# Kernel optimization log

Hardware: AMD Instinct MI355X
Metric: run time of the kernel (lower is better)

## Reference

```python
import jax, jax.numpy as jnp
import numpy as np

V, D, H, NH, C, L = 11, 128, 256, 4, 10, 3  # vocab, d_model, ffn/out dim, heads, classes, layers
DH = D // NH


def setup_inputs() -> dict:
    key = jax.random.key(0)
    ks = jax.random.split(key, 12)
    s = 0.02
    return {
        "support_inputs": jax.random.randint(ks[0], (64, 1024), 0, 11),
        "support_outputs": jax.random.randint(ks[1], (64, 1024), 0, 10),
        "query_input": jax.random.randint(ks[2], (1024,), 0, 11),
        "support_masks": jax.random.randint(ks[3], (64, 1024), 0, 2),
        "emb": (jax.random.normal(ks[4], (V, D)) * s).at[10].set(0.0),  # padding_idx=10
        "Wqkv": jax.random.normal(ks[5], (L, 3 * D, D)) * s,
        "bqkv": jnp.zeros((L, 3 * D)),
        "Wo": jax.random.normal(ks[6], (L, D, D)) * s,
        "bo": jnp.zeros((L, D)),
        "ln1_s": jnp.ones((L, D)), "ln1_b": jnp.zeros((L, D)),
        "W1": jax.random.normal(ks[7], (L, H, D)) * s, "b1": jnp.zeros((L, H)),
        "W2": jax.random.normal(ks[8], (L, D, H)) * s, "b2": jnp.zeros((L, D)),
        "ln2_s": jnp.ones((L, D)), "ln2_b": jnp.zeros((L, D)),
        "Wp": jax.random.normal(ks[9], (H, D)) * s, "bp": jnp.zeros((H,)),
    }


def _ln(x, s, b, eps=1e-5):
    m = x.mean(-1, keepdims=True)
    v = ((x - m) ** 2).mean(-1, keepdims=True)
    return (x - m) / jnp.sqrt(v + eps) * s + b


def _encode(tokens, emb, Wqkv, bqkv, Wo, bo, ln1_s, ln1_b, W1, b1, W2, b2, ln2_s, ln2_b, Wp, bp):
    # PyTorch TransformerEncoderLayer, post-norm (norm_first=False), relu, eval (no dropout)
    x = emb[tokens]  # [B, S, D]
    B, S, _ = x.shape
    scale = 1.0 / jnp.sqrt(jnp.asarray(DH, x.dtype))
    for l in range(L):
        qkv = jnp.einsum('bsd,ed->bse', x, Wqkv[l]) + bqkv[l]
        q, k, v = jnp.split(qkv, 3, axis=-1)
        q = q.reshape(B, S, NH, DH)
        k = k.reshape(B, S, NH, DH)
        v = v.reshape(B, S, NH, DH)
        scores = jnp.einsum('bqhd,bkhd->bhqk', q, k) * scale
        a = jax.nn.softmax(scores, axis=-1)
        o = jnp.einsum('bhqk,bkhd->bqhd', a, v).reshape(B, S, D)
        o = o @ Wo[l].T + bo[l]
        x = _ln(x + o, ln1_s[l], ln1_b[l])
        f = jax.nn.relu(x @ W1[l].T + b1[l]) @ W2[l].T + b2[l]
        x = _ln(x + f, ln2_s[l], ln2_b[l])
    return x @ Wp.T + bp  # [B, S, H]


def reference(support_inputs, support_outputs, query_input, support_masks,
              emb, Wqkv, bqkv, Wo, bo, ln1_s, ln1_b, W1, b1, W2, b2, ln2_s, ln2_b, Wp, bp):
    params = (emb, Wqkv, bqkv, Wo, bo, ln1_s, ln1_b, W1, b1, W2, b2, ln2_s, ln2_b, Wp, bp)
    feat = _encode(support_inputs, *params)  # [N, S, H]
    # vectorized scatter-mean: invalid (masked or cls>=C) tokens go to dummy segment C
    seg = jnp.where((support_masks > 0) & (support_outputs < C), support_outputs, C).reshape(-1)
    flat = feat.reshape(-1, H)
    sums = jax.ops.segment_sum(flat, seg, num_segments=C + 1)[:C]
    cnts = jax.ops.segment_sum(jnp.ones((seg.shape[0],), flat.dtype), seg, num_segments=C + 1)[:C]
    protos = jnp.where(cnts[:, None] > 0, sums / jnp.maximum(cnts, 1.0)[:, None], 0.0)  # [C, H]
    qf = _encode(query_input[None, :], *params)[0]  # [S, H]
    logits = -jnp.sum((qf[:, None, :] - protos[None, :, :]) ** 2, axis=-1)  # -cdist**2, [S, C]
    return logits
```

## Files before the change

### kernel.cpp

```cpp
#include <hip/hip_runtime.h>
#include <hip/hip_bf16.h>

constexpr int D    = 128;
constexpr int HF   = 256;
constexpr int NH   = 4;
constexpr int DH   = 32;
constexpr int NL   = 3;
constexpr int SEQ  = 1024;
constexpr int NB   = 65;
constexpr int NTOK = NB * SEQ;
constexpr int NSUP = 64 * SEQ;
constexpr int NC   = 10;

using u16 = unsigned short;
using u32 = unsigned int;
typedef __bf16 bf16x8 __attribute__((ext_vector_type(8)));
typedef float  f32x4  __attribute__((ext_vector_type(4)));
typedef float  f32x16 __attribute__((ext_vector_type(16)));
typedef u16    u16x4  __attribute__((ext_vector_type(4)));
typedef u16    u16x8  __attribute__((ext_vector_type(8)));
typedef u32    u32x2  __attribute__((ext_vector_type(2)));

static __device__ __forceinline__ u16 f2b(float f) {
  return __builtin_bit_cast(u16, (__bf16)f);
}
static __device__ __forceinline__ float b2f(u16 u) {
  return (float)__builtin_bit_cast(__bf16, u);
}

#define GLOAD16(gsrc, ldst) \
  __builtin_amdgcn_global_load_lds( \
      (const __attribute__((address_space(1))) void*)(gsrc), \
      (__attribute__((address_space(3))) void*)(ldst), 16, 0, 0)

__global__ __launch_bounds__(256) void k_setup(const float* __restrict__ w0,
                                               const float* __restrict__ w1,
                                               const float* __restrict__ w2,
                                               const float* __restrict__ w3,
                                               const float* __restrict__ w4,
                                               u16* __restrict__ wout,
                                               const int* __restrict__ sup,
                                               const int* __restrict__ qry,
                                               const float* __restrict__ emb,
                                               u32* __restrict__ xbw) {
  const int bid = blockIdx.x;
  if (bid < 1664) {
    int i = bid * 256 + threadIdx.x;
    const float* src; int off;
    if      (i < 147456) { src = w0; off = i; }
    else if (i < 196608) { src = w1; off = i - 147456; }
    else if (i < 294912) { src = w2; off = i - 196608; }
    else if (i < 393216) { src = w3; off = i - 294912; }
    else                 { src = w4; off = i - 393216; }
    wout[i] = f2b(src[off]);
  } else {
    int i = (bid - 1664) * 256 + threadIdx.x;
    int tok = i >> 6;
    int d2 = (i & 63) * 2;
    int t = tok < NSUP ? sup[tok] : qry[tok - NSUP];
    float2 e = *(const float2*)(emb + t * D + d2);
    xbw[i] = (u32)f2b(e.x) | ((u32)f2b(e.y) << 16);
  }
}

template<bool RELU, bool BF16OUT>
__global__ __launch_bounds__(256) void k_gemm_mfma(const u16* __restrict__ A,
                                                   const u16* __restrict__ B,
                                                   const float* __restrict__ bias,
                                                   void* __restrict__ Cm,
                                                   int M, int N, int K) {
  extern __shared__ u16 lds[];
  u16* As = lds;
  u16* Bs = lds + 16384;
  const int tid = threadIdx.x;
  const int w = tid >> 6, l = tid & 63;
  const int g = l >> 4, c16 = l & 15;
  const int m0 = blockIdx.y * 128;
  const int n0 = blockIdx.x * 128;

  f32x4 acc[2][8] = {};
  const u16* gA = A + (size_t)(m0 + w * 32 + (l >> 2)) * K + (l & 3) * 8;
  const u16* gB = B + (size_t)(n0 + w * 32 + (l >> 2)) * K + (l & 3) * 8;
  u16* lA = As + w * 32 * 32;
  u16* lB = Bs + w * 32 * 32;

  for (int k0 = 0; k0 < K; k0 += 128) {
    __syncthreads();
    #pragma unroll
    for (int s = 0; s < 4; ++s) {
      const int kk = k0 + s * 32;
      GLOAD16(gA + kk, lA + s * 4096);
      GLOAD16(gA + (size_t)16 * K + kk, lA + s * 4096 + 16 * 32);
      GLOAD16(gB + kk, lB + s * 4096);
      GLOAD16(gB + (size_t)16 * K + kk, lB + s * 4096 + 16 * 32);
    }
    __syncthreads();

    #pragma unroll
    for (int s = 0; s < 4; ++s) {
      const u16* arp = As + s * 4096 + (w * 32 + c16) * 32 + g * 8;
      const u16* brp = Bs + s * 4096 + (size_t)c16 * 32 + g * 8;
      bf16x8 a0 = *(const bf16x8*)(arp);
      bf16x8 a1 = *(const bf16x8*)(arp + 16 * 32);
      #pragma unroll
      for (int nc = 0; nc < 8; ++nc) {
        bf16x8 b = *(const bf16x8*)(brp + nc * 16 * 32);
        acc[0][nc] = __builtin_amdgcn_mfma_f32_16x16x32_bf16(a0, b, acc[0][nc], 0, 0, 0);
        acc[1][nc] = __builtin_amdgcn_mfma_f32_16x16x32_bf16(a1, b, acc[1][nc], 0, 0, 0);
      }
    }
  }

  #pragma unroll
  for (int nc = 0; nc < 8; ++nc) {
    const int n_ = n0 + nc * 16 + c16;
    const float bs = bias[n_];
    #pragma unroll
    for (int mf = 0; mf < 2; ++mf)
      #pragma unroll
      for (int r = 0; r < 4; ++r) {
        const int m_ = m0 + w * 32 + mf * 16 + g * 4 + r;
        float v = acc[mf][nc][r] + bs;
        if (RELU) v = fmaxf(v, 0.f);
        if (BF16OUT) ((u16*)Cm)[(size_t)m_ * N + n_] = f2b(v);
        else         ((float*)Cm)[(size_t)m_ * N + n_] = v;
      }
  }
}

__global__ __launch_bounds__(256) void k_gemm_ln(const u16* __restrict__ A,
                                                 const u16* __restrict__ B,
                                                 const float* __restrict__ bias,
                                                 u16* __restrict__ xres,
                                                 const float* __restrict__ gamma,
                                                 const float* __restrict__ beta,
                                                 int M, int K) {
  extern __shared__ u16 lds[];
  u16* As = lds;
  u16* Bs = lds + 16384;
  const int tid = threadIdx.x;
  const int w = tid >> 6, l = tid & 63;
  const int g = l >> 4, c16 = l & 15;
  const int m0 = blockIdx.x * 128;

  f32x4 acc[2][8] = {};
  const u16* gA = A + (size_t)(m0 + w * 32 + (l >> 2)) * K + (l & 3) * 8;
  const u16* gB = B + (size_t)(w * 32 + (l >> 2)) * K + (l & 3) * 8;
  u16* lA = As + w * 32 * 32;
  u16* lB = Bs + w * 32 * 32;

  for (int k0 = 0; k0 < K; k0 += 128) {
    __syncthreads();
    #pragma unroll
    for (int s = 0; s < 4; ++s) {
      const int kk = k0 + s * 32;
      GLOAD16(gA + kk, lA + s * 4096);
      GLOAD16(gA + (size_t)16 * K + kk, lA + s * 4096 + 16 * 32);
      GLOAD16(gB + kk, lB + s * 4096);
      GLOAD16(gB + (size_t)16 * K + kk, lB + s * 4096 + 16 * 32);
    }
    __syncthreads();

    #pragma unroll
    for (int s = 0; s < 4; ++s) {
      const u16* arp = As + s * 4096 + (w * 32 + c16) * 32 + g * 8;
      const u16* brp = Bs + s * 4096 + (size_t)c16 * 32 + g * 8;
      bf16x8 a0 = *(const bf16x8*)(arp);
      bf16x8 a1 = *(const bf16x8*)(arp + 16 * 32);
      #pragma unroll
      for (int nc = 0; nc < 8; ++nc) {
        bf16x8 b = *(const bf16x8*)(brp + nc * 16 * 32);
        acc[0][nc] = __builtin_amdgcn_mfma_f32_16x16x32_bf16(a0, b, acc[0][nc], 0, 0, 0);
        acc[1][nc] = __builtin_amdgcn_mfma_f32_16x16x32_bf16(a1, b, acc[1][nc], 0, 0, 0);
      }
    }
  }

  float bsv[8], gms[8], bts[8];
  #pragma unroll
  for (int nc = 0; nc < 8; ++nc) {
    int col = nc * 16 + c16;
    bsv[nc] = bias[col]; gms[nc] = gamma[col]; bts[nc] = beta[col];
  }

  #pragma unroll
  for (int mf = 0; mf < 2; ++mf)
    #pragma unroll
    for (int r = 0; r < 4; ++r) {
      const int row = m0 + w * 32 + mf * 16 + g * 4 + r;
      u16* xrow = xres + (size_t)row * 128;
      float v[8];
      float s = 0.f, q = 0.f;
      #pragma unroll
      for (int nc = 0; nc < 8; ++nc) {
        float t = acc[mf][nc][r] + bsv[nc] + b2f(xrow[nc * 16 + c16]);
        v[nc] = t; s += t; q += t * t;
      }
      #pragma unroll
      for (int off = 8; off; off >>= 1) {
        s += __shfl_xor(s, off);
        q += __shfl_xor(q, off);
      }
      float mean = s * (1.f / 128.f);
      float var  = q * (1.f / 128.f) - mean * mean;
      float invn = 1.f / sqrtf(var + 1e-5f);
      #pragma unroll
      for (int nc = 0; nc < 8; ++nc)
        xrow[nc * 16 + c16] = f2b((v[nc] - mean) * invn * gms[nc] + bts[nc]);
    }
}

__global__ __launch_bounds__(256) void k_attn_mfma(const u16* __restrict__ qkvb,
                                                   u16* __restrict__ out) {
  const int i = blockIdx.x;
  const int b = (i & 7) + (((i >> 3) >> 4) << 3);
  if (b >= NB) return;
  const int qt = (i >> 3) & 15;
  const int tid = threadIdx.x;
  const int h = tid >> 6;
  const int l = tid & 63;
  const int q5 = l & 31;
  const int hi = l >> 5;
  const int qbase = qt * 64;

  __shared__ u16 VtAll[4][2304];
  u16* Vt = VtAll[h];
  u32* Vtw = (u32*)Vt;

  const size_t tok0 = (size_t)b * SEQ;
  constexpr float KSL = 0.25500446f;

  const u16* qrowA = qkvb + (tok0 + qbase + q5) * 384 + h * 32 + hi * 8;
  bf16x8 qA0 = *(const bf16x8*)(qrowA);
  bf16x8 qA1 = *(const bf16x8*)(qrowA + 16);
  const u16* qrowB = qrowA + (size_t)32 * 384;
  bf16x8 qB0 = *(const bf16x8*)(qrowB);
  bf16x8 qB1 = *(const bf16x8*)(qrowB + 16);

  f32x16 accA = {}, accB = {};
  float lsA = 0.f, lsB = 0.f;

  const u16* kbase = qkvb + tok0 * 384 + 128 + h * 32 + (size_t)q5 * 384 + hi * 8;
  const u16* vbase = qkvb + tok0 * 384 + 256 + h * 32 + hi * 16;
  const f32x16 z16 = {};

  for (int kt = 0; kt < SEQ; kt += 64) {
    const u16* vr0 = vbase + (size_t)(kt + q5 * 2) * 384;
    const u16* vr1 = vr0 + 384;
    u16x8 a_lo = *(const u16x8*)(vr0);
    u16x8 a_hi = *(const u16x8*)(vr0 + 8);
    u16x8 b_lo = *(const u16x8*)(vr1);
    u16x8 b_hi = *(const u16x8*)(vr1 + 8);
    const u16* kr = kbase + (size_t)kt * 384;
    bf16x8 k00 = *(const bf16x8*)(kr);
    bf16x8 k01 = *(const bf16x8*)(kr + 16);
    bf16x8 k10 = *(const bf16x8*)(kr + (size_t)32 * 384);
    bf16x8 k11 = *(const bf16x8*)(kr + (size_t)32 * 384 + 16);

    #pragma unroll
    for (int j = 0; j < 8; ++j) {
      Vtw[(hi * 16 + j) * 36 + q5]     = (u32)a_lo[j] | ((u32)b_lo[j] << 16);
      Vtw[(hi * 16 + 8 + j) * 36 + q5] = (u32)a_hi[j] | ((u32)b_hi[j] << 16);
    }

    f32x16 sA0 = __builtin_amdgcn_mfma_f32_32x32x16_bf16(k00, qA0, z16, 0, 0, 0);
    sA0 = __builtin_amdgcn_mfma_f32_32x32x16_bf16(k01, qA1, sA0, 0, 0, 0);
    f32x16 sA1 = __builtin_amdgcn_mfma_f32_32x32x16_bf16(k10, qA0, z16, 0, 0, 0);
    sA1 = __builtin_amdgcn_mfma_f32_32x32x16_bf16(k11, qA1, sA1, 0, 0, 0);
    f32x16 sB0 = __builtin_amdgcn_mfma_f32_32x32x16_bf16(k00, qB0, z16, 0, 0, 0);
    sB0 = __builtin_amdgcn_mfma_f32_32x32x16_bf16(k01, qB1, sB0, 0, 0, 0);
    f32x16 sB1 = __builtin_amdgcn_mfma_f32_32x32x16_bf16(k10, qB0, z16, 0, 0, 0);
    sB1 = __builtin_amdgcn_mfma_f32_32x32x16_bf16(k11, qB1, sB1, 0, 0, 0);

    u32 pkA0[8], pkA1[8], pkB0[8], pkB1[8];
    {
      float ps0 = 0.f, ps1 = 0.f;
      #pragma unroll
      for (int mi = 0; mi < 8; ++mi) {
        float e0 = __builtin_amdgcn_exp2f(sA0[2 * mi] * KSL);
        float e1 = __builtin_amdgcn_exp2f(sA0[2 * mi + 1] * KSL);
        float e2 = __builtin_amdgcn_exp2f(sA1[2 * mi] * KSL);
        float e3 = __builtin_amdgcn_exp2f(sA1[2 * mi + 1] * KSL);
        ps0 += e0 + e1; ps1 += e2 + e3;
        pkA0[mi] = (u32)f2b(e0) | ((u32)f2b(e1) << 16);
        pkA1[mi] = (u32)f2b(e2) | ((u32)f2b(e3) << 16);
      }
      lsA += ps0 + ps1;
    }
    {
      float ps0 = 0.f, ps1 = 0.f;
      #pragma unroll
      for (int mi = 0; mi < 8; ++mi) {
        float e0 = __builtin_amdgcn_exp2f(sB0[2 * mi] * KSL);
        float e1 = __builtin_amdgcn_exp2f(sB0[2 * mi + 1] * KSL);
        float e2 = __builtin_amdgcn_exp2f(sB1[2 * mi] * KSL);
        float e3 = __builtin_amdgcn_exp2f(sB1[2 * mi + 1] * KSL);
        ps0 += e0 + e1; ps1 += e2 + e3;
        pkB0[mi] = (u32)f2b(e0) | ((u32)f2b(e1) << 16);
        pkB1[mi] = (u32)f2b(e2) | ((u32)f2b(e3) << 16);
      }
      lsB += ps0 + ps1;
    }

    #pragma unroll
    for (int t = 0; t < 2; ++t) {
      #pragma unroll
      for (int hh = 0; hh < 2; ++hh) {
        bf16x8 vf = *(const bf16x8*)(Vt + (size_t)q5 * 72 + t * 32 + hh * 16 + hi * 8);
        {
          u32 a0w = t ? pkA1[4 * hh + 0] : pkA0[4 * hh + 0];
          u32 a1w = t ? pkA1[4 * hh + 1] : pkA0[4 * hh + 1];
          u32 a2w = t ? pkA1[4 * hh + 2] : pkA0[4 * hh + 2];
          u32 a3w = t ? pkA1[4 * hh + 3] : pkA0[4 * hh + 3];
          u32x2 r02 = __builtin_amdgcn_permlane32_swap(a0w, a2w, false, false);
          u32x2 r13 = __builtin_amdgcn_permlane32_swap(a1w, a3w, false, false);
          union { u32 w[4]; bf16x8 v; } pf;
          pf.w[0] = r02.x; pf.w[1] = r13.x; pf.w[2] = r02.y; pf.w[3] = r13.y;
          accA = __builtin_amdgcn_mfma_f32_32x32x16_bf16(vf, pf.v, accA, 0, 0, 0);
        }
        {
          u32 a0w = t ? pkB1[4 * hh + 0] : pkB0[4 * hh + 0];
          u32 a1w = t ? pkB1[4 * hh + 1] : pkB0[4 * hh + 1];
          u32 a2w = t ? pkB1[4 * hh + 2] : pkB0[4 * hh + 2];
          u32 a3w = t ? pkB1[4 * hh + 3] : pkB0[4 * hh + 3];
          u32x2 r02 = __builtin_amdgcn_permlane32_swap(a0w, a2w, false, false);
          u32x2 r13 = __builtin_amdgcn_permlane32_swap(a1w, a3w, false, false);
          union { u32 w[4]; bf16x8 v; } pf;
          pf.w[0] = r02.x; pf.w[1] = r13.x; pf.w[2] = r02.y; pf.w[3] = r13.y;
          accB = __builtin_amdgcn_mfma_f32_32x32x16_bf16(vf, pf.v, accB, 0, 0, 0);
        }
      }
    }
  }

  lsA += __shfl_xor(lsA, 32);
  lsB += __shfl_xor(lsB, 32);
  float invA = 1.f / lsA, invB = 1.f / lsB;
  u16* orowA = out + (tok0 + qbase + q5) * 128 + h * 32 + hi * 4;
  u16* orowB = orowA + (size_t)32 * 128;
  #pragma unroll
  for (int a = 0; a < 4; ++a) {
    u16x4 stA, stB;
    #pragma unroll
    for (int j = 0; j < 4; ++j) {
      stA[j] = f2b(accA[a * 4 + j] * invA);
      stB[j] = f2b(accB[a * 4 + j] * invB);
    }
    *(u16x4*)(orowA + a * 8) = stA;
    *(u16x4*)(orowB + a * 8) = stB;
  }
}

__global__ __launch_bounds__(256) void k_proto_accum(const u16* __restrict__ feat,
                                                     const int* __restrict__ cls,
                                                     const int* __restrict__ msk,
                                                     float* __restrict__ psum,
                                                     int* __restrict__ pcnt) {
  __shared__ float ls[NC][HF];
  __shared__ int lc[NC];
  int tid = threadIdx.x;
  #pragma unroll
  for (int c = 0; c < NC; ++c) ls[c][tid] = 0.f;
  if (tid < NC) lc[tid] = 0;
  __syncthreads();
  int t0 = blockIdx.x * 256;
  for (int t = t0; t < t0 + 256; ++t) {
    int cl = cls[t];
    int mk = msk[t];
    if (mk > 0 && cl < NC) {
      ls[cl][tid] += b2f(feat[(size_t)t * HF + tid]);
      if (tid == 0) lc[cl]++;
    }
  }
  __syncthreads();
  for (int c = 0; c < NC; ++c) atomicAdd(&psum[c * HF + tid], ls[c][tid]);
  if (tid < NC) atomicAdd(&pcnt[tid], lc[tid]);
}

__global__ __launch_bounds__(256) void k_logits(const u16* __restrict__ feat,
                                                const float* __restrict__ psum,
                                                const int* __restrict__ pcnt,
                                                float* __restrict__ out) {
  __shared__ float pl[NC * HF];
  const int tid = threadIdx.x;
  #pragma unroll
  for (int j = 0; j < NC * HF / 256; ++j) {
    int idx = j * 256 + tid;
    int c = idx >> 8;
    int n = pcnt[c];
    pl[idx] = (n > 0) ? psum[idx] / (float)n : 0.f;
  }
  __syncthreads();

  int i = blockIdx.x * 256 + tid;
  if (i >= SEQ * NC) return;
  int s = i / NC, c = i % NC;
  const u16* qf = feat + (size_t)(NSUP + s) * HF;
  const float* pr = pl + c * HF;
  float acc = 0.f;
  for (int hh = 0; hh < 32; ++hh) {
    u16x8 v = *(const u16x8*)(qf + hh * 8);
    #pragma unroll
    for (int j = 0; j < 8; ++j) {
      float d = b2f(v[j]) - pr[hh * 8 + j];
      acc += d * d;
    }
  }
  out[i] = -acc;
}

extern "C" void kernel_launch(void* const* d_in, const int* in_sizes, int n_in,
                              void* d_out, int out_size, void* d_ws, size_t ws_size,
                              hipStream_t stream) {
  const int*   sup_in  = (const int*)d_in[0];
  const int*   sup_out = (const int*)d_in[1];
  const int*   qry_in  = (const int*)d_in[2];
  const int*   sup_msk = (const int*)d_in[3];
  const float* emb     = (const float*)d_in[4];
  const float* Wqkv    = (const float*)d_in[5];
  const float* bqkv    = (const float*)d_in[6];
  const float* Wo      = (const float*)d_in[7];
  const float* bo      = (const float*)d_in[8];
  const float* ln1s    = (const float*)d_in[9];
  const float* ln1b    = (const float*)d_in[10];
  const float* W1      = (const float*)d_in[11];
  const float* b1      = (const float*)d_in[12];
  const float* W2      = (const float*)d_in[13];
  const float* b2      = (const float*)d_in[14];
  const float* ln2s    = (const float*)d_in[15];
  const float* ln2b    = (const float*)d_in[16];
  const float* Wp      = (const float*)d_in[17];
  const float* bp      = (const float*)d_in[18];

  u16* xb = (u16*)d_ws;
  u16* yb = xb + (size_t)NTOK * D;
  u16* U  = yb + (size_t)NTOK * D;
  u16* qkvb  = U;
  u16* midb  = U;
  u16* featb = U;
  u16* wqkvb = U + (size_t)NTOK * 384;
  u16* wob   = wqkvb + 3 * 384 * 128;
  u16* w1b   = wob + 3 * 128 * 128;
  u16* w2b   = w1b + 3 * 256 * 128;
  u16* wpb   = w2b + 3 * 128 * 256;
  float* psum  = (float*)(((size_t)(wpb + 256 * 128) + 15) & ~(size_t)15);
  int*   pcnt  = (int*)(psum + NC * HF);
  float* outp = (float*)d_out;

  constexpr size_t GEMM_LDS = 65536;

  hipMemsetAsync(psum, 0, NC * HF * sizeof(float) + 16 * sizeof(int), stream);

  k_setup<<<dim3(1664 + 16640), 256, 0, stream>>>(
      Wqkv, Wo, W1, W2, Wp, wqkvb, sup_in, qry_in, emb, (u32*)xb);

  for (int l = 0; l < NL; ++l) {
    k_gemm_mfma<false, true><<<dim3(3, NTOK / 128), 256, GEMM_LDS, stream>>>(
        xb, wqkvb + (size_t)l * 384 * 128, bqkv + l * 384, qkvb, NTOK, 384, D);
    k_attn_mfma<<<dim3(1152), 256, 0, stream>>>(qkvb, yb);
    k_gemm_ln<<<dim3(NTOK / 128), 256, GEMM_LDS, stream>>>(
        yb, wob + (size_t)l * 128 * 128, bo + l * D, xb,
        ln1s + l * D, ln1b + l * D, NTOK, D);
    k_gemm_mfma<true, true><<<dim3(2, NTOK / 128), 256, GEMM_LDS, stream>>>(
        xb, w1b + (size_t)l * 256 * 128, b1 + l * HF, midb, NTOK, HF, D);
    k_gemm_ln<<<dim3(NTOK / 128), 256, GEMM_LDS, stream>>>(
        midb, w2b + (size_t)l * 128 * 256, b2 + l * D, xb,
        ln2s + l * D, ln2b + l * D, NTOK, HF);
  }

  k_gemm_mfma<false, true><<<dim3(2, NTOK / 128), 256, GEMM_LDS, stream>>>(
      xb, wpb, bp, featb, NTOK, HF, D);
  k_proto_accum<<<dim3(NSUP / 256), 256, 0, stream>>>(featb, sup_out, sup_msk, psum, pcnt);
  k_logits<<<dim3((SEQ * NC + 255) / 256), 256, 0, stream>>>(featb, psum, pcnt, outp);
}
```

Baseline: 636.6 us.

## Load A tile once per block and loop over all N tiles in GEMM

The bf16 MFMA GEMM (K=128) now assigns each block a 128-row strip of M and iterates over every 128-column N tile inside the kernel. The A tile is loaded into LDS once and reused across the N tiles, instead of separate blocks each reloading A for their own N tile. This removes the redundant A traffic, but it cuts the grid size by 2-3x and serialises the N tiles within a block. It also hardcodes K to 128.

After: 673.5 us. 1.06x slower.

```diff
diff --git a/kernel.cpp b/kernel.cpp
--- a/kernel.cpp
+++ b/kernel.cpp
@@ -68,34 +68,37 @@
                                                    const u16* __restrict__ B,
                                                    const float* __restrict__ bias,
                                                    void* __restrict__ Cm,
-                                                   int M, int N, int K) {
+                                                   int M, int N) {
+  constexpr int K = 128;
   extern __shared__ u16 lds[];
   u16* As = lds;
   u16* Bs = lds + 16384;
   const int tid = threadIdx.x;
   const int w = tid >> 6, l = tid & 63;
   const int g = l >> 4, c16 = l & 15;
-  const int m0 = blockIdx.y * 128;
-  const int n0 = blockIdx.x * 128;
-
-  f32x4 acc[2][8] = {};
+  const int m0 = blockIdx.x * 128;
+
   const u16* gA = A + (size_t)(m0 + w * 32 + (l >> 2)) * K + (l & 3) * 8;
-  const u16* gB = B + (size_t)(n0 + w * 32 + (l >> 2)) * K + (l & 3) * 8;
+  const u16* gB = B + (size_t)(w * 32 + (l >> 2)) * K + (l & 3) * 8;
   u16* lA = As + w * 32 * 32;
   u16* lB = Bs + w * 32 * 32;
 
-  for (int k0 = 0; k0 < K; k0 += 128) {
+  #pragma unroll
+  for (int s = 0; s < 4; ++s) {
+    GLOAD16(gA + s * 32, lA + s * 4096);
+    GLOAD16(gA + (size_t)16 * K + s * 32, lA + s * 4096 + 16 * 32);
+  }
+
+  for (int n0 = 0; n0 < N; n0 += 128) {
     __syncthreads();
     #pragma unroll
     for (int s = 0; s < 4; ++s) {
-      const int kk = k0 + s * 32;
-      GLOAD16(gA + kk, lA + s * 4096);
-      GLOAD16(gA + (size_t)16 * K + kk, lA + s * 4096 + 16 * 32);
-      GLOAD16(gB + kk, lB + s * 4096);
-      GLOAD16(gB + (size_t)16 * K + kk, lB + s * 4096 + 16 * 32);
+      GLOAD16(gB + (size_t)n0 * K + s * 32, lB + s * 4096);
+      GLOAD16(gB + (size_t)(n0 + 16) * K + s * 32, lB + s * 4096 + 16 * 32);
     }
     __syncthreads();
 
+    f32x4 acc[2][8] = {};
     #pragma unroll
     for (int s = 0; s < 4; ++s) {
       const u16* arp = As + s * 4096 + (w * 32 + c16) * 32 + g * 8;
@@ -109,22 +112,22 @@
         acc[1][nc] = __builtin_amdgcn_mfma_f32_16x16x32_bf16(a1, b, acc[1][nc], 0, 0, 0);
       }
     }
-  }
-
-  #pragma unroll
-  for (int nc = 0; nc < 8; ++nc) {
-    const int n_ = n0 + nc * 16 + c16;
-    const float bs = bias[n_];
-    #pragma unroll
-    for (int mf = 0; mf < 2; ++mf)
-      #pragma unroll
-      for (int r = 0; r < 4; ++r) {
-        const int m_ = m0 + w * 32 + mf * 16 + g * 4 + r;
-        float v = acc[mf][nc][r] + bs;
-        if (RELU) v = fmaxf(v, 0.f);
-        if (BF16OUT) ((u16*)Cm)[(size_t)m_ * N + n_] = f2b(v);
-        else         ((float*)Cm)[(size_t)m_ * N + n_] = v;
-      }
+
+    #pragma unroll
+    for (int nc = 0; nc < 8; ++nc) {
+      const int n_ = n0 + nc * 16 + c16;
+      const float bs = bias[n_];
+      #pragma unroll
+      for (int mf = 0; mf < 2; ++mf)
+        #pragma unroll
+        for (int r = 0; r < 4; ++r) {
+          const int m_ = m0 + w * 32 + mf * 16 + g * 4 + r;
+          float v = acc[mf][nc][r] + bs;
+          if (RELU) v = fmaxf(v, 0.f);
+          if (BF16OUT) ((u16*)Cm)[(size_t)m_ * N + n_] = f2b(v);
+          else         ((float*)Cm)[(size_t)m_ * N + n_] = v;
+        }
+    }
   }
 }
 
@@ -455,21 +458,21 @@
       Wqkv, Wo, W1, W2, Wp, wqkvb, sup_in, qry_in, emb, (u32*)xb);
 
   for (int l = 0; l < NL; ++l) {
-    k_gemm_mfma<false, true><<<dim3(3, NTOK / 128), 256, GEMM_LDS, stream>>>(
-        xb, wqkvb + (size_t)l * 384 * 128, bqkv + l * 384, qkvb, NTOK, 384, D);
+    k_gemm_mfma<false, true><<<dim3(NTOK / 128), 256, GEMM_LDS, stream>>>(
+        xb, wqkvb + (size_t)l * 384 * 128, bqkv + l * 384, qkvb, NTOK, 384);
     k_attn_mfma<<<dim3(1152), 256, 0, stream>>>(qkvb, yb);
     k_gemm_ln<<<dim3(NTOK / 128), 256, GEMM_LDS, stream>>>(
         yb, wob + (size_t)l * 128 * 128, bo + l * D, xb,
         ln1s + l * D, ln1b + l * D, NTOK, D);
-    k_gemm_mfma<true, true><<<dim3(2, NTOK / 128), 256, GEMM_LDS, stream>>>(
-        xb, w1b + (size_t)l * 256 * 128, b1 + l * HF, midb, NTOK, HF, D);
+    k_gemm_mfma<true, true><<<dim3(NTOK / 128), 256, GEMM_LDS, stream>>>(
+        xb, w1b + (size_t)l * 256 * 128, b1 + l * HF, midb, NTOK, HF);
     k_gemm_ln<<<dim3(NTOK / 128), 256, GEMM_LDS, stream>>>(
         midb, w2b + (size_t)l * 128 * 256, b2 + l * D, xb,
         ln2s + l * D, ln2b + l * D, NTOK, HF);
   }
 
-  k_gemm_mfma<false, true><<<dim3(2, NTOK / 128), 256, GEMM_LDS, stream>>>(
-      xb, wpb, bp, featb, NTOK, HF, D);
+  k_gemm_mfma<false, true><<<dim3(NTOK / 128), 256, GEMM_LDS, stream>>>(
+      xb, wpb, bp, featb, NTOK, HF);
   k_proto_accum<<<dim3(NSUP / 256), 256, 0, stream>>>(featb, sup_out, sup_msk, psum, pcnt);
   k_logits<<<dim3((SEQ * NC + 255) / 256), 256, 0, stream>>>(featb, psum, pcnt, outp);
 }
```
